# Kernel optimization log

Measured on AMD Instinct MI355X. Metric: run time of the kernel, lower is better.

Reference implementation:

```python
import jax, jax.numpy as jnp
import numpy as np

N_NODES = 100000
N_EDGES = 150000
D_IN = 512
D_HID = 512
N_GRAPHS = 64


def setup_inputs() -> dict:
    key = jax.random.key(0)
    ks = jax.random.split(key, 12)
    x = jax.random.normal(ks[0], (N_NODES, D_IN), dtype=jnp.float32)
    edge_index = jax.random.randint(ks[1], (2, N_EDGES), 0, N_NODES, dtype=jnp.int64)
    batch = jnp.sort(jax.random.randint(ks[2], (N_NODES,), 0, N_GRAPHS, dtype=jnp.int64))
    s1 = 1.0 / np.sqrt(D_IN)
    s2 = 1.0 / np.sqrt(D_HID)
    # GINConv layer 1: MLP([D_IN, D_HID, D_HID])
    W1a = jax.random.uniform(ks[3], (D_IN, D_HID), jnp.float32, -s1, s1)
    b1a = jax.random.uniform(ks[4], (D_HID,), jnp.float32, -s1, s1)
    W1b = jax.random.uniform(ks[5], (D_HID, D_HID), jnp.float32, -s2, s2)
    b1b = jax.random.uniform(ks[6], (D_HID,), jnp.float32, -s2, s2)
    # GINConv layer 2 (out_channels=1): MLP([D_HID, 1, 1])
    W2a = jax.random.uniform(ks[7], (D_HID, 1), jnp.float32, -s2, s2)
    b2a = jax.random.uniform(ks[8], (1,), jnp.float32, -s2, s2)
    W2b = jax.random.uniform(ks[9], (1, 1), jnp.float32, -1.0, 1.0)
    b2b = jax.random.uniform(ks[10], (1,), jnp.float32, -1.0, 1.0)
    return {"x": x, "edge_index": edge_index, "batch": batch,
            "W1a": W1a, "b1a": b1a, "W1b": W1b, "b1b": b1b,
            "W2a": W2a, "b2a": b2a, "W2b": W2b, "b2b": b2b}


def _gin_conv(h, src, dst, Wa, ba, Wb, bb):
    # sum-aggregate neighbor features, add (1+eps)*x with eps=0, then MLP
    agg = jax.ops.segment_sum(h[src], dst, num_segments=N_NODES)  # [N, d]
    z = agg + h
    z = jnp.maximum(jnp.dot(z, Wa) + ba, 0.0)  # Linear -> ReLU
    return jnp.dot(z, Wb) + bb                  # Linear (plain last)


def reference(x, edge_index, batch, W1a, b1a, W1b, b1b, W2a, b2a, W2b, b2b):
    src, dst = edge_index[0], edge_index[1]
    h = _gin_conv(x, src, dst, W1a, b1a, W1b, b1b)
    h = jnp.maximum(h, 0.0)  # inter-layer activation (not applied after last layer)
    h = _gin_conv(h, src, dst, W2a, b2a, W2b, b2b)  # [N, 1]
    # global mean pool over graph assignment
    sums = jax.ops.segment_sum(h, batch, num_segments=N_GRAPHS)  # [G, 1]
    cnt = jax.ops.segment_sum(jnp.ones((N_NODES, 1), h.dtype), batch, num_segments=N_GRAPHS)
    return sums / jnp.maximum(cnt, 1.0)
```

## Files before the change

kernel.cpp:

```cpp
#include <hip/hip_runtime.h>
#include <hip/hip_bf16.h>

#define N_NODES_C 100000
#define N_EDGES_C 150000
#define DC 512
#define NG 64

typedef float f32x4 __attribute__((ext_vector_type(4)));
typedef short s16x8 __attribute__((ext_vector_type(8)));
typedef short s16x4 __attribute__((ext_vector_type(4)));

__device__ __forceinline__ short f2bf(float f) {
    union { float f; unsigned u; } c; c.f = f;
    unsigned r = c.u + 0x7fffu + ((c.u >> 16) & 1u);
    return (short)(r >> 16);
}
__device__ __forceinline__ float bf2f(short v) {
    union { unsigned u; float f; } c;
    c.u = ((unsigned)(unsigned short)v) << 16;
    return c.f;
}


__global__ void zero_k(float* s, float* aggs, int* cnt, float* gsum, float* gcnt) {
    int i = blockIdx.x * 256 + threadIdx.x;
    if (i < N_NODES_C) { s[i] = 0.f; aggs[i] = 0.f; cnt[i] = 0; }
    if (i < NG) { gsum[i] = 0.f; gcnt[i] = 0.f; }
}

__global__ void transpose_w(const float* __restrict__ in, short* __restrict__ out) {
    __shared__ float tile[32][33];
    int tx = threadIdx.x & 31;
    int ty = threadIdx.x >> 5;
    int k0 = blockIdx.y * 32;
    int n0 = blockIdx.x * 32;
#pragma unroll
    for (int i = 0; i < 4; ++i)
        tile[ty + i * 8][tx] = in[(size_t)(k0 + ty + i * 8) * DC + n0 + tx];
    __syncthreads();
#pragma unroll
    for (int i = 0; i < 4; ++i)
        out[(size_t)(n0 + ty + i * 8) * DC + k0 + tx] = f2bf(tile[tx][ty + i * 8]);
}


__global__ void hist_k(const int* __restrict__ ei, int* __restrict__ cnt) {
    int e = blockIdx.x * 256 + threadIdx.x;
    if (e < N_EDGES_C) atomicAdd(&cnt[ei[N_EDGES_C + e]], 1);
}

__global__ void scan1_k(const int* __restrict__ cnt, int* __restrict__ off,
                        int* __restrict__ bsum) {
    __shared__ int sh[1024];
    int tid = threadIdx.x;
    int i = blockIdx.x * 1024 + tid;
    int v = (i < N_NODES_C) ? cnt[i] : 0;
    sh[tid] = v;
    __syncthreads();
    for (int d = 1; d < 1024; d <<= 1) {
        int t = (tid >= d) ? sh[tid - d] : 0;
        __syncthreads();
        sh[tid] += t;
        __syncthreads();
    }
    if (i < N_NODES_C) off[i] = sh[tid] - v;
    if (tid == 1023) bsum[blockIdx.x] = sh[1023];
}

#define NSCAN_BLK 98

__global__ void scan2_k(int* __restrict__ bsum) {
    __shared__ int sh[128];
    int tid = threadIdx.x;
    int v = (tid < NSCAN_BLK) ? bsum[tid] : 0;
    sh[tid] = v;
    __syncthreads();
    for (int d = 1; d < 128; d <<= 1) {
        int t = (tid >= d) ? sh[tid - d] : 0;
        __syncthreads();
        sh[tid] += t;
        __syncthreads();
    }
    if (tid < NSCAN_BLK) bsum[tid] = sh[tid] - v;
}

__global__ void scan3_k(int* __restrict__ off, const int* __restrict__ bsum) {
    int i = blockIdx.x * 1024 + threadIdx.x;
    if (i < N_NODES_C) off[i] += bsum[blockIdx.x];
}

__global__ void place_k(const int* __restrict__ ei, int* __restrict__ off,
                        int* __restrict__ ssrc) {
    int e = blockIdx.x * 256 + threadIdx.x;
    if (e < N_EDGES_C) {
        int d = ei[N_EDGES_C + e];
        int p = atomicAdd(&off[d], 1);
        ssrc[p] = ei[e];
    }
}

__global__ void gather_relu_k(const short* __restrict__ y, const int* __restrict__ off,
                              const int* __restrict__ ssrc, const float* __restrict__ b1a,
                              short* __restrict__ z1) {
    int node = blockIdx.x * 4 + (threadIdx.x >> 6);
    if (node >= N_NODES_C) return;
    int t = threadIdx.x & 63;
    const int col = t * 8;
    int beg = (node == 0) ? 0 : off[node - 1];
    int end = off[node];
    s16x8 own = *(const s16x8*)(y + (size_t)node * DC + col);
    float acc[8];
#pragma unroll
    for (int q = 0; q < 8; ++q) acc[q] = bf2f(own[q]);
    int j = beg;
    for (; j + 2 <= end; j += 2) {
        int s0 = ssrc[j];
        int s1 = ssrc[j + 1];
        s16x8 r0 = *(const s16x8*)(y + (size_t)s0 * DC + col);
        s16x8 r1 = *(const s16x8*)(y + (size_t)s1 * DC + col);
#pragma unroll
        for (int q = 0; q < 8; ++q) acc[q] += bf2f(r0[q]) + bf2f(r1[q]);
    }
    if (j < end) {
        int s0 = ssrc[j];
        s16x8 r0 = *(const s16x8*)(y + (size_t)s0 * DC + col);
#pragma unroll
        for (int q = 0; q < 8; ++q) acc[q] += bf2f(r0[q]);
    }
    f32x4 bv0 = *(const f32x4*)(b1a + col);
    f32x4 bv1 = *(const f32x4*)(b1a + col + 4);
    s16x8 o;
    o[0] = f2bf(fmaxf(acc[0] + bv0.x, 0.f));
    o[1] = f2bf(fmaxf(acc[1] + bv0.y, 0.f));
    o[2] = f2bf(fmaxf(acc[2] + bv0.z, 0.f));
    o[3] = f2bf(fmaxf(acc[3] + bv0.w, 0.f));
    o[4] = f2bf(fmaxf(acc[4] + bv1.x, 0.f));
    o[5] = f2bf(fmaxf(acc[5] + bv1.y, 0.f));
    o[6] = f2bf(fmaxf(acc[6] + bv1.z, 0.f));
    o[7] = f2bf(fmaxf(acc[7] + bv1.w, 0.f));
    *(s16x8*)(z1 + (size_t)node * DC + col) = o;
}


__global__ void edge_scalar(const int* __restrict__ ei, const float* __restrict__ s,
                            float* __restrict__ aggs) {
    int e = blockIdx.x * 256 + threadIdx.x;
    if (e < N_EDGES_C) atomicAdd(&aggs[ei[N_EDGES_C + e]], s[ei[e]]);
}

__global__ void node_pool(const float* __restrict__ s, const float* __restrict__ aggs,
                          const int* __restrict__ batch, const float* __restrict__ b2a,
                          float* __restrict__ gsum, float* __restrict__ gcnt) {
    __shared__ float ls[NG], lc[NG];
    int t = threadIdx.x;
    if (t < NG) { ls[t] = 0.f; lc[t] = 0.f; }
    __syncthreads();
    int i = blockIdx.x * 256 + t;
    if (i < N_NODES_C) {
        float z2 = fmaxf(aggs[i] + s[i] + b2a[0], 0.0f);
        int g = batch[i];
        atomicAdd(&ls[g], z2);
        atomicAdd(&lc[g], 1.0f);
    }
    __syncthreads();
    if (t < NG && lc[t] != 0.f) {
        atomicAdd(&gsum[t], ls[t]);
        atomicAdd(&gcnt[t], lc[t]);
    }
}

__global__ void finalize_k(const float* gsum, const float* gcnt, const float* w2b,
                           const float* b2b, float* out) {
    int g = threadIdx.x;
    if (g < NG) {
        float c = fmaxf(gcnt[g], 1.0f);
        out[g] = gsum[g] / c * w2b[0] + b2b[0];
    }
}

#define BM 128
#define BN 128
#define BK 32
#define LDK 40

template <int ASRC, int EPI>
__global__ __launch_bounds__(256, 2) void gemm_k(const void* __restrict__ Ap,
                                                 const short* __restrict__ Bt,
                                                 const float* __restrict__ bias,
                                                 short* __restrict__ Cout,
                                                 const float* __restrict__ w2a,
                                                 float* __restrict__ s_out) {
    __shared__ alignas(16) short As[BM * LDK];
    __shared__ alignas(16) short Bs[BN * LDK];

    const int tid  = threadIdx.x;
    const int brow = blockIdx.y * BM;
    const int bcol = blockIdx.x * BN;

    const int lane = tid & 63;
    const int wr   = (tid >> 7) * 64;
    const int wc   = ((tid >> 6) & 1) * 64;
    const int lr   = lane & 15;
    const int lk   = (lane >> 4) * 8;

    f32x4 acc[4][4] = {};

    const int str = tid >> 1;
    const int skk = (tid & 1) * 16;
    int arow = brow + str;
    if (arow >= N_NODES_C) arow = N_NODES_C - 1;

    const short* bgp = Bt + (size_t)(bcol + str) * DC + skk;

    for (int kt = 0; kt < DC / BK; ++kt) {
        const int k0 = kt * BK;
        short areg[16];
        if constexpr (ASRC == 0) {
            const float* ap = (const float*)Ap + (size_t)arow * DC + k0 + skk;
            f32x4 a0 = *(const f32x4*)(ap + 0);
            f32x4 a1 = *(const f32x4*)(ap + 4);
            f32x4 a2 = *(const f32x4*)(ap + 8);
            f32x4 a3 = *(const f32x4*)(ap + 12);
            areg[0]  = f2bf(a0.x); areg[1]  = f2bf(a0.y); areg[2]  = f2bf(a0.z); areg[3]  = f2bf(a0.w);
            areg[4]  = f2bf(a1.x); areg[5]  = f2bf(a1.y); areg[6]  = f2bf(a1.z); areg[7]  = f2bf(a1.w);
            areg[8]  = f2bf(a2.x); areg[9]  = f2bf(a2.y); areg[10] = f2bf(a2.z); areg[11] = f2bf(a2.w);
            areg[12] = f2bf(a3.x); areg[13] = f2bf(a3.y); areg[14] = f2bf(a3.z); areg[15] = f2bf(a3.w);
        } else {
            const short* ap = (const short*)Ap + (size_t)arow * DC + k0 + skk;
            *(s16x8*)&areg[0] = *(const s16x8*)(ap + 0);
            *(s16x8*)&areg[8] = *(const s16x8*)(ap + 8);
        }
        s16x8 b0 = *(const s16x8*)(bgp + k0);
        s16x8 b1 = *(const s16x8*)(bgp + k0 + 8);

        __syncthreads();
        *(s16x8*)&As[str * LDK + skk + 0] = *(s16x8*)&areg[0];
        *(s16x8*)&As[str * LDK + skk + 8] = *(s16x8*)&areg[8];
        *(s16x8*)&Bs[str * LDK + skk + 0] = b0;
        *(s16x8*)&Bs[str * LDK + skk + 8] = b1;
        __syncthreads();

        s16x8 af[4], bfr[4];
#pragma unroll
        for (int mi = 0; mi < 4; ++mi)
            af[mi] = *(const s16x8*)&As[(wr + mi * 16 + lr) * LDK + lk];
#pragma unroll
        for (int ni = 0; ni < 4; ++ni)
            bfr[ni] = *(const s16x8*)&Bs[(wc + ni * 16 + lr) * LDK + lk];
#pragma unroll
        for (int mi = 0; mi < 4; ++mi)
#pragma unroll
            for (int ni = 0; ni < 4; ++ni)
                acc[mi][ni] = __builtin_amdgcn_mfma_f32_16x16x32_bf16(af[mi], bfr[ni],
                                                                      acc[mi][ni], 0, 0, 0);
    }

    const int rb = brow + wr + (lane >> 4) * 4;
    const int cb = bcol + wc + lr;

    if constexpr (EPI == 0 || EPI == 2) {
        float bv[4] = {0.f, 0.f, 0.f, 0.f};
        if constexpr (EPI == 0) {
#pragma unroll
            for (int ni = 0; ni < 4; ++ni) bv[ni] = bias[cb + ni * 16];
        }
#pragma unroll
        for (int mi = 0; mi < 4; ++mi) {
#pragma unroll
            for (int r = 0; r < 4; ++r) {
                int row = rb + mi * 16 + r;
                if (row < N_NODES_C) {
#pragma unroll
                    for (int ni = 0; ni < 4; ++ni) {
                        float v = acc[mi][ni][r] + bv[ni];
                        if constexpr (EPI == 0) v = fmaxf(v, 0.0f);
                        Cout[(size_t)row * DC + cb + ni * 16] = f2bf(v);
                    }
                }
            }
        }
    } else {
        float bv[4], wv[4];
#pragma unroll
        for (int ni = 0; ni < 4; ++ni) {
            bv[ni] = bias[cb + ni * 16];
            wv[ni] = w2a[cb + ni * 16];
        }
#pragma unroll
        for (int mi = 0; mi < 4; ++mi) {
#pragma unroll
            for (int r = 0; r < 4; ++r) {
                float sum = 0.f;
#pragma unroll
                for (int ni = 0; ni < 4; ++ni) {
                    float v = fmaxf(acc[mi][ni][r] + bv[ni], 0.0f);
                    sum += v * wv[ni];
                }
#pragma unroll
                for (int off = 1; off < 16; off <<= 1) sum += __shfl_xor(sum, off, 64);
                int row = rb + mi * 16 + r;
                if (lr == 0 && row < N_NODES_C) atomicAdd(&s_out[row], sum);
            }
        }
    }
}


extern "C" void kernel_launch(void* const* d_in, const int* in_sizes, int n_in,
                              void* d_out, int out_size, void* d_ws, size_t ws_size,
                              hipStream_t stream) {
    const float* x     = (const float*)d_in[0];
    const int*   ei    = (const int*)d_in[1];
    const int*   batch = (const int*)d_in[2];
    const float* W1a   = (const float*)d_in[3];
    const float* b1a   = (const float*)d_in[4];
    const float* W1b   = (const float*)d_in[5];
    const float* b1b   = (const float*)d_in[6];
    const float* W2a   = (const float*)d_in[7];
    const float* b2a   = (const float*)d_in[8];
    const float* W2b   = (const float*)d_in[9];
    const float* b2b   = (const float*)d_in[10];
    float* out = (float*)d_out;

    char* w = (char*)d_ws;
    short* y    = (short*)(w);
    short* z1   = (short*)(w + 102400000);
    short* WT1  = (short*)(w + 204800000);
    short* WT2  = (short*)(w + 205324288);
    float* sbuf = (float*)(w + 205848576);
    float* aggs = (float*)(w + 206248576);
    int*   cnt  = (int*)  (w + 206648576);
    int*   offb = (int*)  (w + 207048576);
    int*   ssrc = (int*)  (w + 207448576);
    int*   bsum = (int*)  (w + 208048576);
    float* gsum = (float*)(w + 208049088);
    float* gcnt = (float*)(w + 208049344);

    zero_k<<<391, 256, 0, stream>>>(sbuf, aggs, cnt, gsum, gcnt);
    transpose_w<<<dim3(16, 16), 256, 0, stream>>>(W1a, WT1);
    transpose_w<<<dim3(16, 16), 256, 0, stream>>>(W1b, WT2);

    hist_k<<<586, 256, 0, stream>>>(ei, cnt);
    scan1_k<<<NSCAN_BLK, 1024, 0, stream>>>(cnt, offb, bsum);
    scan2_k<<<1, 128, 0, stream>>>(bsum);
    scan3_k<<<NSCAN_BLK, 1024, 0, stream>>>(offb, bsum);
    place_k<<<586, 256, 0, stream>>>(ei, offb, ssrc);

    gemm_k<0, 2><<<dim3(4, 782), 256, 0, stream>>>(x, WT1, nullptr, y, nullptr, nullptr);
    gather_relu_k<<<25000, 256, 0, stream>>>(y, offb, ssrc, b1a, z1);
    gemm_k<1, 1><<<dim3(4, 782), 256, 0, stream>>>(z1, WT2, b1b, nullptr, W2a, sbuf);

    edge_scalar<<<586, 256, 0, stream>>>(ei, sbuf, aggs);
    node_pool<<<391, 256, 0, stream>>>(sbuf, aggs, batch, b2a, gsum, gcnt);
    finalize_k<<<1, 64, 0, stream>>>(gsum, gcnt, W2b, b2b, out);
}
```

Baseline: 340.9 us.

## Pre-convert x to bf16 and stage GEMM tiles via direct global-to-LDS loads

```diff
diff --git a/kernel.cpp b/kernel.cpp
--- a/kernel.cpp
+++ b/kernel.cpp
@@ -8,7 +8,7 @@
 
 typedef float f32x4 __attribute__((ext_vector_type(4)));
 typedef short s16x8 __attribute__((ext_vector_type(8)));
-typedef short s16x4 __attribute__((ext_vector_type(4)));
+typedef unsigned int u32;
 
 __device__ __forceinline__ short f2bf(float f) {
     union { float f; unsigned u; } c; c.f = f;
@@ -21,11 +21,32 @@
     return c.f;
 }
 
+__device__ __forceinline__ void gload16(const void* g, void* l) {
+    __builtin_amdgcn_global_load_lds((const __attribute__((address_space(1))) u32*)g,
+                                     (__attribute__((address_space(3))) u32*)l,
+                                     16, 0, 0);
+}
+
 
 __global__ void zero_k(float* s, float* aggs, int* cnt, float* gsum, float* gcnt) {
     int i = blockIdx.x * 256 + threadIdx.x;
     if (i < N_NODES_C) { s[i] = 0.f; aggs[i] = 0.f; cnt[i] = 0; }
     if (i < NG) { gsum[i] = 0.f; gcnt[i] = 0.f; }
+}
+
+__global__ void cvt_k(const float* __restrict__ x, short* __restrict__ xb, int n8) {
+    int i = blockIdx.x * 256 + threadIdx.x;
+    int stride = gridDim.x * 256;
+    const f32x4* xs = (const f32x4*)x;
+    s16x8* o = (s16x8*)xb;
+    for (; i < n8; i += stride) {
+        f32x4 a = xs[i * 2];
+        f32x4 b = xs[i * 2 + 1];
+        s16x8 r;
+        r[0] = f2bf(a.x); r[1] = f2bf(a.y); r[2] = f2bf(a.z); r[3] = f2bf(a.w);
+        r[4] = f2bf(b.x); r[5] = f2bf(b.y); r[6] = f2bf(b.z); r[7] = f2bf(b.w);
+        o[i] = r;
+    }
 }
 
 __global__ void transpose_w(const float* __restrict__ in, short* __restrict__ out) {
@@ -181,72 +202,67 @@
 #define BM 128
 #define BN 128
 #define BK 32
-#define LDK 40
-
-template <int ASRC, int EPI>
-__global__ __launch_bounds__(256, 2) void gemm_k(const void* __restrict__ Ap,
+#define NRB 782
+#define NCB 4
+#define NWG (NRB * NCB)
+#define WG_PER_XCD (NWG / 8)
+
+template <int EPI>
+__global__ __launch_bounds__(256, 2) void gemm_k(const short* __restrict__ A,
                                                  const short* __restrict__ Bt,
                                                  const float* __restrict__ bias,
                                                  short* __restrict__ Cout,
                                                  const float* __restrict__ w2a,
                                                  float* __restrict__ s_out) {
-    __shared__ alignas(16) short As[BM * LDK];
-    __shared__ alignas(16) short Bs[BN * LDK];
-
-    const int tid  = threadIdx.x;
-    const int brow = blockIdx.y * BM;
-    const int bcol = blockIdx.x * BN;
-
+    __shared__ alignas(16) short As[BM * BK];
+    __shared__ alignas(16) short Bs[BN * BK];
+
+    const int tid = threadIdx.x;
+    const int bid = blockIdx.x;
+    const int lin = (bid & 7) * WG_PER_XCD + (bid >> 3);
+    const int brow = (lin >> 2) * BM;
+    const int bcol = (lin & 3) * BN;
+
+    const int w    = tid >> 6;
     const int lane = tid & 63;
-    const int wr   = (tid >> 7) * 64;
-    const int wc   = ((tid >> 6) & 1) * 64;
+    const int wr   = (w >> 1) * 64;
+    const int wc   = (w & 1) * 64;
     const int lr   = lane & 15;
     const int lk   = (lane >> 4) * 8;
 
     f32x4 acc[4][4] = {};
 
-    const int str = tid >> 1;
-    const int skk = (tid & 1) * 16;
-    int arow = brow + str;
-    if (arow >= N_NODES_C) arow = N_NODES_C - 1;
-
-    const short* bgp = Bt + (size_t)(bcol + str) * DC + skk;
+    const int srow = lane >> 2;
+    const int scol = (lane & 3) * 8;
+    int ar0 = brow + w * 32 + srow;
+    int ar1 = ar0 + 16;
+    if (ar0 >= N_NODES_C) ar0 = N_NODES_C - 1;
+    if (ar1 >= N_NODES_C) ar1 = N_NODES_C - 1;
+    const short* ag0 = A + (size_t)ar0 * DC + scol;
+    const short* ag1 = A + (size_t)ar1 * DC + scol;
+    const short* bg0 = Bt + (size_t)(bcol + w * 32 + srow) * DC + scol;
+    const short* bg1 = bg0 + (size_t)16 * DC;
+    short* al0 = &As[(w * 32) * BK];
+    short* al1 = &As[(w * 32 + 16) * BK];
+    short* bl0 = &Bs[(w * 32) * BK];
+    short* bl1 = &Bs[(w * 32 + 16) * BK];
 
     for (int kt = 0; kt < DC / BK; ++kt) {
         const int k0 = kt * BK;
-        short areg[16];
-        if constexpr (ASRC == 0) {
-            const float* ap = (const float*)Ap + (size_t)arow * DC + k0 + skk;
-            f32x4 a0 = *(const f32x4*)(ap + 0);
-            f32x4 a1 = *(const f32x4*)(ap + 4);
-            f32x4 a2 = *(const f32x4*)(ap + 8);
-            f32x4 a3 = *(const f32x4*)(ap + 12);
-            areg[0]  = f2bf(a0.x); areg[1]  = f2bf(a0.y); areg[2]  = f2bf(a0.z); areg[3]  = f2bf(a0.w);
-            areg[4]  = f2bf(a1.x); areg[5]  = f2bf(a1.y); areg[6]  = f2bf(a1.z); areg[7]  = f2bf(a1.w);
-            areg[8]  = f2bf(a2.x); areg[9]  = f2bf(a2.y); areg[10] = f2bf(a2.z); areg[11] = f2bf(a2.w);
-            areg[12] = f2bf(a3.x); areg[13] = f2bf(a3.y); areg[14] = f2bf(a3.z); areg[15] = f2bf(a3.w);
-        } else {
-            const short* ap = (const short*)Ap + (size_t)arow * DC + k0 + skk;
-            *(s16x8*)&areg[0] = *(const s16x8*)(ap + 0);
-            *(s16x8*)&areg[8] = *(const s16x8*)(ap + 8);
-        }
-        s16x8 b0 = *(const s16x8*)(bgp + k0);
-        s16x8 b1 = *(const s16x8*)(bgp + k0 + 8);
-
-        __syncthreads();
-        *(s16x8*)&As[str * LDK + skk + 0] = *(s16x8*)&areg[0];
-        *(s16x8*)&As[str * LDK + skk + 8] = *(s16x8*)&areg[8];
-        *(s16x8*)&Bs[str * LDK + skk + 0] = b0;
-        *(s16x8*)&Bs[str * LDK + skk + 8] = b1;
+        __syncthreads();
+        gload16(ag0 + k0, al0);
+        gload16(ag1 + k0, al1);
+        gload16(bg0 + k0, bl0);
+        gload16(bg1 + k0, bl1);
         __syncthreads();
 
         s16x8 af[4], bfr[4];
 #pragma unroll
         for (int mi = 0; mi < 4; ++mi)
-            af[mi] = *(const s16x8*)&As[(wr + mi * 16 + lr) * LDK + lk];
+            af[mi] = *(const s16x8*)&As[(wr + mi * 16 + lr) * BK + lk];
 #pragma unroll
         for (int ni = 0; ni < 4; ++ni)
-            bfr[ni] = *(const s16x8*)&Bs[(wc + ni * 16 + lr) * LDK + lk];
+            bfr[ni] = *(const s16x8*)&Bs[(wc + ni * 16 + lr) * BK + lk];
 #pragma unroll
         for (int mi = 0; mi < 4; ++mi)
 #pragma unroll
@@ -258,12 +274,7 @@
     const int rb = brow + wr + (lane >> 4) * 4;
     const int cb = bcol + wc + lr;
 
-    if constexpr (EPI == 0 || EPI == 2) {
-        float bv[4] = {0.f, 0.f, 0.f, 0.f};
-        if constexpr (EPI == 0) {
-#pragma unroll
-            for (int ni = 0; ni < 4; ++ni) bv[ni] = bias[cb + ni * 16];
-        }
+    if constexpr (EPI == 2) {
 #pragma unroll
         for (int mi = 0; mi < 4; ++mi) {
 #pragma unroll
@@ -271,11 +282,8 @@
                 int row = rb + mi * 16 + r;
                 if (row < N_NODES_C) {
 #pragma unroll
-                    for (int ni = 0; ni < 4; ++ni) {
-                        float v = acc[mi][ni][r] + bv[ni];
-                        if constexpr (EPI == 0) v = fmaxf(v, 0.0f);
-                        Cout[(size_t)row * DC + cb + ni * 16] = f2bf(v);
-                    }
+                    for (int ni = 0; ni < 4; ++ni)
+                        Cout[(size_t)row * DC + cb + ni * 16] = f2bf(acc[mi][ni][r]);
                 }
             }
         }
@@ -323,8 +331,8 @@
     float* out = (float*)d_out;
 
     char* w = (char*)d_ws;
-    short* y    = (short*)(w);
-    short* z1   = (short*)(w + 102400000);
+    short* buf0 = (short*)(w);
+    short* y    = (short*)(w + 102400000);
     short* WT1  = (short*)(w + 204800000);
     short* WT2  = (short*)(w + 205324288);
     float* sbuf = (float*)(w + 205848576);
@@ -340,15 +348,17 @@
     transpose_w<<<dim3(16, 16), 256, 0, stream>>>(W1a, WT1);
     transpose_w<<<dim3(16, 16), 256, 0, stream>>>(W1b, WT2);
 
+    cvt_k<<<2048, 256, 0, stream>>>(x, buf0, N_NODES_C * DC / 8);
+
     hist_k<<<586, 256, 0, stream>>>(ei, cnt);
     scan1_k<<<NSCAN_BLK, 1024, 0, stream>>>(cnt, offb, bsum);
     scan2_k<<<1, 128, 0, stream>>>(bsum);
     scan3_k<<<NSCAN_BLK, 1024, 0, stream>>>(offb, bsum);
     place_k<<<586, 256, 0, stream>>>(ei, offb, ssrc);
 
-    gemm_k<0, 2><<<dim3(4, 782), 256, 0, stream>>>(x, WT1, nullptr, y, nullptr, nullptr);
-    gather_relu_k<<<25000, 256, 0, stream>>>(y, offb, ssrc, b1a, z1);
-    gemm_k<1, 1><<<dim3(4, 782), 256, 0, stream>>>(z1, WT2, b1b, nullptr, W2a, sbuf);
+    gemm_k<2><<<NWG, 256, 0, stream>>>(buf0, WT1, nullptr, y, nullptr, nullptr);
+    gather_relu_k<<<25000, 256, 0, stream>>>(y, offb, ssrc, b1a, buf0);
+    gemm_k<1><<<NWG, 256, 0, stream>>>(buf0, WT2, b1b, nullptr, W2a, sbuf);
 
     edge_scalar<<<586, 256, 0, stream>>>(ei, sbuf, aggs);
     node_pool<<<391, 256, 0, stream>>>(sbuf, aggs, batch, b2a, gsum, gcnt);
```

Result: faster. 312.4 us (-8.3%).
